# Performance work log

Hardware: AMD Instinct MI355X
Metric: run time of the kernel (lower is better)

Reference implementation:

```python
import jax, jax.numpy as jnp
import numpy as np

B, T, D = 2, 1024, 1024
H, DK = 16, 64  # n_head, d_k; inner dim = H*DK = D
INV_SQRT_DK = 1.0 / float(np.sqrt(DK))


def setup_inputs() -> dict:
    key = jax.random.key(0)
    ks = jax.random.split(key, 16)
    init = lambda k, shape: (jax.random.normal(k, shape, dtype=jnp.float32) * 0.02)
    return {
        "query": jax.random.normal(ks[0], (B, T, D), dtype=jnp.float32),
        "key": jax.random.normal(ks[1], (B, T, D), dtype=jnp.float32),
        "value": jax.random.normal(ks[2], (B, T, D), dtype=jnp.float32),
        "pos_k": jax.random.normal(ks[3], (T, T, DK), dtype=jnp.float32),
        "pos_v": jax.random.normal(ks[4], (T, T, DK), dtype=jnp.float32),
        "mask": jnp.ones((B, T, T), dtype=jnp.int32),
        "relative_attention_bias": jax.random.normal(ks[5], (1, H, T, T), dtype=jnp.float32),
        "Wq": init(ks[6], (D, D)), "bq": init(ks[7], (D,)),
        "Wk": init(ks[8], (D, D)), "bk": init(ks[9], (D,)),
        "Wv": init(ks[10], (D, D)), "bv": init(ks[11], (D,)),
        "Wo": init(ks[12], (D, D)), "bo": init(ks[13], (D,)),
    }


def reference(query, key, value, pos_k, pos_v, mask, relative_attention_bias,
              Wq, bq, Wk, bk, Wv, bv, Wo, bo):
    nb = query.shape[0]
    # projections -> (B, H, T, DK); q pre-scaled by 1/sqrt(d_k)
    q = (query @ Wq + bq).reshape(nb, -1, H, DK).transpose(0, 2, 1, 3) * INV_SQRT_DK
    k = (key @ Wk + bk).reshape(nb, -1, H, DK).transpose(0, 2, 1, 3)
    v = (value @ Wv + bv).reshape(nb, -1, H, DK).transpose(0, 2, 1, 3)

    # content scores + relative-position key scores (B, H, T, S)
    A = jnp.einsum('bhtd,bhsd->bhts', q, k)
    Bp = jnp.einsum('bhtd,tsd->bhts', q, pos_k)
    scores = A + Bp + relative_attention_bias

    # masked softmax: mask (B, T, S) -> invalid where mask == 0
    inv = (mask[:, None, :, :] == 0)  # (B, 1, T, S)
    scores = jnp.where(inv, -jnp.inf, scores)
    attn = jax.nn.softmax(scores, axis=-1)
    attn = jnp.where(inv, 0.0, attn)

    # value aggregation + relative-position value term
    x = jnp.einsum('bhts,bhsd->bhtd', attn, v)
    x = x + jnp.einsum('bhts,tsd->bhtd', attn, pos_v)

    x = x.transpose(0, 2, 1, 3).reshape(nb, -1, H * DK)  # (B, T, D)
    return x @ Wo + bo
```

## Files before the change

### kernel.cpp

```cpp
#include <hip/hip_runtime.h>


#define DEV __device__ __forceinline__

typedef short bf16x8 __attribute__((ext_vector_type(8)));
typedef float f32x4 __attribute__((ext_vector_type(4)));

DEV short f2b(float f) {
  unsigned u = __builtin_bit_cast(unsigned, f);
  u = (u + 0x7FFFu + ((u >> 16) & 1u)) >> 16;
  return (short)u;
}
DEV float b2f(short s) {
  unsigned u = ((unsigned)(unsigned short)s) << 16;
  return __builtin_bit_cast(float, u);
}

#define MFMA(a, b, c) __builtin_amdgcn_mfma_f32_16x16x32_bf16(a, b, c, 0, 0, 0)

DEV void gload16(const void* g, void* l) {
  __builtin_amdgcn_global_load_lds(
      (const __attribute__((address_space(1))) void*)g,
      (__attribute__((address_space(3))) void*)l, 16, 0, 0);
}

__global__ __launch_bounds__(256) void k_cvt3(
    const float* __restrict__ a, const float* __restrict__ b, const float* __restrict__ c,
    short* __restrict__ oa, short* __restrict__ ob, short* __restrict__ oc) {
  const float* src = blockIdx.y == 0 ? a : (blockIdx.y == 1 ? b : c);
  short* dst = blockIdx.y == 0 ? oa : (blockIdx.y == 1 ? ob : oc);
  size_t i = ((size_t)blockIdx.x * 256 + threadIdx.x) * 8;
  float4 p0 = *(const float4*)(src + i);
  float4 p1 = *(const float4*)(src + i + 4);
  bf16x8 o;
  o[0] = f2b(p0.x); o[1] = f2b(p0.y); o[2] = f2b(p0.z); o[3] = f2b(p0.w);
  o[4] = f2b(p1.x); o[5] = f2b(p1.y); o[6] = f2b(p1.z); o[7] = f2b(p1.w);
  *(bf16x8*)(dst + i) = o;
}

__global__ __launch_bounds__(256) void k_wtrans4(
    const float* __restrict__ w0, const float* __restrict__ w1,
    const float* __restrict__ w2, const float* __restrict__ w3,
    short* __restrict__ o0, short* __restrict__ o1,
    short* __restrict__ o2, short* __restrict__ o3) {
  const float* src; short* dst;
  switch (blockIdx.z) {
    case 0: src = w0; dst = o0; break;
    case 1: src = w1; dst = o1; break;
    case 2: src = w2; dst = o2; break;
    default: src = w3; dst = o3;
  }
  __shared__ short LW[64][74];
  const int tid = threadIdx.x;
  const int k0 = blockIdx.y * 64, n0 = blockIdx.x * 64;
  {
    int c4 = (tid & 15) * 4;
#pragma unroll
    for (int i = 0; i < 4; ++i) {
      int r = (tid >> 4) + i * 16;
      float4 v = *(const float4*)(src + (size_t)(k0 + r) * 1024 + n0 + c4);
      LW[r][c4 + 0] = f2b(v.x); LW[r][c4 + 1] = f2b(v.y);
      LW[r][c4 + 2] = f2b(v.z); LW[r][c4 + 3] = f2b(v.w);
    }
  }
  __syncthreads();
  {
    int n = tid >> 2, kb = (tid & 3) * 16;
#pragma unroll
    for (int j2 = 0; j2 < 2; ++j2) {
      int kk = kb + j2 * 8;
      bf16x8 o;
#pragma unroll
      for (int j = 0; j < 8; ++j) o[j] = LW[kk + j][n];
      *(bf16x8*)(dst + (size_t)(n0 + n) * 1024 + k0 + kk) = o;
    }
  }
}

__global__ __launch_bounds__(256) void k_qkv(
    const short* __restrict__ Ain, const short* __restrict__ WT,
    const float* __restrict__ bq, const float* __restrict__ bk,
    const float* __restrict__ bv,
    short* __restrict__ qo, short* __restrict__ ko, short* __restrict__ vTo) {
  __shared__ short As[128 * 32];
  __shared__ short Bs[128 * 32];
  __shared__ short LW[128][136];
  const int tid = threadIdx.x;
  const int w = tid >> 6, l = tid & 63, lg = l >> 4, lr = l & 15;
  const int wm = w >> 1, wn = w & 1;
  const int n0 = blockIdx.x * 128;
  const int m0 = blockIdx.y * 128;
  const int seg = m0 >> 11;
  const int mseg = m0 & 2047;
  const short* Abase = Ain + ((size_t)m0 << 10);
  const short* Bbase = WT + ((size_t)seg << 20) + ((size_t)n0 << 10);
  const int srow = l >> 2, scol8 = (l & 3) * 8;
  f32x4 acc[4][4] = {};
  for (int k0 = 0; k0 < 1024; k0 += 32) {
#pragma unroll
    for (int c = 0; c < 2; ++c) {
      int chunk = w * 2 + c;
      int row = chunk * 16 + srow;
      gload16(Abase + (size_t)row * 1024 + k0 + scol8, &As[chunk * 512]);
      gload16(Bbase + (size_t)row * 1024 + k0 + scol8, &Bs[chunk * 512]);
    }
    __syncthreads();
    bf16x8 af[4], bf[4];
#pragma unroll
    for (int i = 0; i < 4; ++i) af[i] = *(const bf16x8*)&As[(wm * 64 + i * 16 + lr) * 32 + lg * 8];
#pragma unroll
    for (int i = 0; i < 4; ++i) bf[i] = *(const bf16x8*)&Bs[(wn * 64 + i * 16 + lr) * 32 + lg * 8];
#pragma unroll
    for (int mi = 0; mi < 4; ++mi)
#pragma unroll
      for (int ni = 0; ni < 4; ++ni) acc[mi][ni] = MFMA(af[mi], bf[ni], acc[mi][ni]);
    __syncthreads();
  }
  const float* bias = seg == 0 ? bq : (seg == 1 ? bk : bv);
  const float scale = seg == 0 ? 0.125f : 1.0f;
  float bvals[4];
#pragma unroll
  for (int ni = 0; ni < 4; ++ni) bvals[ni] = bias[n0 + wn * 64 + ni * 16 + lr];
#pragma unroll
  for (int mi = 0; mi < 4; ++mi)
#pragma unroll
    for (int ni = 0; ni < 4; ++ni)
#pragma unroll
      for (int r = 0; r < 4; ++r)
        LW[wm * 64 + mi * 16 + lg * 4 + r][wn * 64 + ni * 16 + lr] =
            f2b((acc[mi][ni][r] + bvals[ni]) * scale);
  __syncthreads();
  if (seg < 2) {
    short* dst = seg == 0 ? qo : ko;
    int r = tid >> 1, half = tid & 1;
    int m = mseg + r, b = m >> 10, t = m & 1023;
#pragma unroll
    for (int g = 0; g < 8; ++g) {
      int n = n0 + half * 64 + g * 8;
      int h = n >> 6, dk = n & 63;
      bf16x8 o = *(const bf16x8*)&LW[r][half * 64 + g * 8];
      *(bf16x8*)(dst + (((size_t)(b * 16 + h) * 1024 + t) << 6) + dk) = o;
    }
  } else {
    int dkc = tid & 127, th = tid >> 7;
    int n = n0 + dkc, h = n >> 6, dk = n & 63;
    int b = mseg >> 10;
    int tbase = (mseg & 1023) + th * 64;
#pragma unroll
    for (int g = 0; g < 8; ++g) {
      bf16x8 o;
#pragma unroll
      for (int e = 0; e < 8; ++e) o[e] = LW[th * 64 + g * 8 + e][dkc];
      *(bf16x8*)(vTo + (((size_t)(b * 16 + h) * 64 + dk) << 10) + tbase + g * 8) = o;
    }
  }
}

__global__ __launch_bounds__(256) void k_posk_bias(
    const short* __restrict__ q, const float* __restrict__ pos_k,
    const float* __restrict__ rab, const int* __restrict__ mask,
    short* __restrict__ S) {
  const int t = blockIdx.y;
  const int tid = threadIdx.x;
  const int w = tid >> 6, l = tid & 63, lg = l >> 4, lr = l & 15;
  const int s0 = blockIdx.x * 256 + w * 64;
  __shared__ short LW[4][32][74];
  bf16x8 af[2][2];
#pragma unroll
  for (int mi = 0; mi < 2; ++mi)
#pragma unroll
    for (int kk = 0; kk < 2; ++kk) {
      int bh = mi * 16 + lr;
      af[mi][kk] = *(const bf16x8*)(q + ((size_t)bh * 1024 + t) * 64 + kk * 32 + lg * 8);
    }
  f32x4 acc[2][4] = {};
#pragma unroll
  for (int ni = 0; ni < 4; ++ni) {
    int s = s0 + ni * 16 + lr;
#pragma unroll
    for (int kk = 0; kk < 2; ++kk) {
      const float* pk = pos_k + ((size_t)t * 1024 + s) * 64 + kk * 32 + lg * 8;
      const float4 p0 = *(const float4*)pk;
      const float4 p1 = *(const float4*)(pk + 4);
      bf16x8 bfr;
      bfr[0] = f2b(p0.x); bfr[1] = f2b(p0.y); bfr[2] = f2b(p0.z); bfr[3] = f2b(p0.w);
      bfr[4] = f2b(p1.x); bfr[5] = f2b(p1.y); bfr[6] = f2b(p1.z); bfr[7] = f2b(p1.w);
#pragma unroll
      for (int mi = 0; mi < 2; ++mi) acc[mi][ni] = MFMA(af[mi][kk], bfr, acc[mi][ni]);
    }
  }
#pragma unroll
  for (int ni = 0; ni < 4; ++ni) {
    int s = s0 + ni * 16 + lr;
    int msk0 = mask[(size_t)t * 1024 + s];
    int msk1 = mask[(size_t)(1024 + t) * 1024 + s];
#pragma unroll
    for (int r = 0; r < 4; ++r) {
      int h = lg * 4 + r;
      float bv = rab[((size_t)h * 1024 + t) * 1024 + s];
      float v0 = acc[0][ni][r] + bv;
      float v1 = acc[1][ni][r] + bv;
      if (msk0 == 0) v0 = -1e30f;
      if (msk1 == 0) v1 = -1e30f;
      LW[w][h][ni * 16 + lr] = f2b(v0);
      LW[w][16 + h][ni * 16 + lr] = f2b(v1);
    }
  }
#pragma unroll
  for (int rr = 0; rr < 4; ++rr) {
    int row = (l >> 3) + rr * 8;
    int s8 = (l & 7) * 8;
    bf16x8 o = *(const bf16x8*)&LW[w][row][s8];
    *(bf16x8*)(S + ((size_t)row * 1024 + t) * 1024 + s0 + s8) = o;
  }
}

__global__ __launch_bounds__(512, 4) void k_attn_softmax(
    const short* __restrict__ q, const short* __restrict__ kmat,
    short* __restrict__ S) {
  const int bh = blockIdx.y;
  const int tid = threadIdx.x;
  const int w = tid >> 6, l = tid & 63, lg = l >> 4, lr = l & 15;
  const int wm = w >> 2, wn = w & 3;
  const int t0 = blockIdx.x * 32 + wm * 16;
  const int scol = wn * 256;
  __shared__ short LS[8][16][266];
  __shared__ float redA[32][4];
  __shared__ float redB[32][4];

  short* sb = (short*)(S + ((size_t)bh * 1024 + t0) * 1024 + scol);
  const int r2 = l >> 5, c16 = (l & 31) * 8;
#pragma unroll
  for (int rr = 0; rr < 8; ++rr) {
    int row = rr * 2 + r2;
    *(bf16x8*)&LS[w][row][c16] = *(const bf16x8*)(sb + (size_t)row * 1024 + c16);
  }

  bf16x8 af[2];
#pragma unroll
  for (int kk = 0; kk < 2; ++kk)
    af[kk] = *(const bf16x8*)(q + ((size_t)bh * 1024 + (t0 + lr)) * 64 + kk * 32 + lg * 8);

  f32x4 acc[16];
#pragma unroll
  for (int ni = 0; ni < 16; ++ni) {
    int s = scol + ni * 16 + lr;
    const short* kp = kmat + ((size_t)bh * 1024 + s) * 64 + lg * 8;
    bf16x8 b0 = *(const bf16x8*)kp;
    bf16x8 b1 = *(const bf16x8*)(kp + 32);
    f32x4 a = {};
    a = MFMA(af[0], b0, a);
    a = MFMA(af[1], b1, a);
    acc[ni] = a;
  }
#pragma unroll
  for (int ni = 0; ni < 16; ++ni)
#pragma unroll
    for (int r = 0; r < 4; ++r) acc[ni][r] += b2f(LS[w][lg * 4 + r][ni * 16 + lr]);

  float pm[4];
#pragma unroll
  for (int r = 0; r < 4; ++r) {
    float m = acc[0][r];
#pragma unroll
    for (int ni = 1; ni < 16; ++ni) m = fmaxf(m, acc[ni][r]);
    m = fmaxf(m, __shfl_xor(m, 1));
    m = fmaxf(m, __shfl_xor(m, 2));
    m = fmaxf(m, __shfl_xor(m, 4));
    m = fmaxf(m, __shfl_xor(m, 8));
    pm[r] = m;
  }
  if (lr == 0) {
#pragma unroll
    for (int r = 0; r < 4; ++r) redA[wm * 16 + lg * 4 + r][wn] = pm[r];
  }
  __syncthreads();
  float rowm[4];
#pragma unroll
  for (int r = 0; r < 4; ++r) {
    int row = wm * 16 + lg * 4 + r;
    rowm[r] = fmaxf(fmaxf(redA[row][0], redA[row][1]), fmaxf(redA[row][2], redA[row][3]));
  }
  float rs[4];
#pragma unroll
  for (int r = 0; r < 4; ++r) {
    float sum = 0.f;
#pragma unroll
    for (int ni = 0; ni < 16; ++ni) {
      float e = __expf(acc[ni][r] - rowm[r]);
      acc[ni][r] = e;
      sum += e;
    }
    sum += __shfl_xor(sum, 1);
    sum += __shfl_xor(sum, 2);
    sum += __shfl_xor(sum, 4);
    sum += __shfl_xor(sum, 8);
    rs[r] = sum;
  }
  if (lr == 0) {
#pragma unroll
    for (int r = 0; r < 4; ++r) redB[wm * 16 + lg * 4 + r][wn] = rs[r];
  }
  __syncthreads();
#pragma unroll
  for (int r = 0; r < 4; ++r) {
    int row = wm * 16 + lg * 4 + r;
    float inv = 1.0f / (redB[row][0] + redB[row][1] + redB[row][2] + redB[row][3]);
#pragma unroll
    for (int ni = 0; ni < 16; ++ni) LS[w][lg * 4 + r][ni * 16 + lr] = f2b(acc[ni][r] * inv);
  }
#pragma unroll
  for (int rr = 0; rr < 8; ++rr) {
    int row = rr * 2 + r2;
    bf16x8 o = *(const bf16x8*)&LS[w][row][c16];
    *(bf16x8*)(sb + (size_t)row * 1024 + c16) = o;
  }
}

__global__ __launch_bounds__(256) void k_posv(
    const short* __restrict__ S, const float* __restrict__ pos_v,
    short* __restrict__ X0h) {
  const int t = blockIdx.x;
  const int tid = threadIdx.x;
  const int w = tid >> 6, l = tid & 63, lg = l >> 4, lr = l & 15;
  const int mi = w >> 1;
  const int nb = (w & 1) * 2;
  __shared__ short pv[256][66];
  f32x4 acc[2] = {};
  const int srow = tid >> 4;
  const int dk4 = (tid & 15) * 4;
  for (int c = 0; c < 4; ++c) {
    int sc = c * 256;
    if (c) __syncthreads();
#pragma unroll
    for (int it = 0; it < 16; ++it) {
      int s = srow + it * 16;
      float4 p = *(const float4*)(pos_v + ((size_t)t * 1024 + sc + s) * 64 + dk4);
      unsigned p0 = (unsigned)(unsigned short)f2b(p.x) | ((unsigned)(unsigned short)f2b(p.y) << 16);
      unsigned p1 = (unsigned)(unsigned short)f2b(p.z) | ((unsigned)(unsigned short)f2b(p.w) << 16);
      *(unsigned*)&pv[s][dk4] = p0;
      *(unsigned*)&pv[s][dk4 + 2] = p1;
    }
    __syncthreads();
    const int bh = mi * 16 + lr;
#pragma unroll
    for (int kk = 0; kk < 8; ++kk) {
      bf16x8 afr = *(const bf16x8*)(S + ((size_t)bh * 1024 + t) * 1024 + sc + kk * 32 + lg * 8);
#pragma unroll
      for (int ni = 0; ni < 2; ++ni) {
        int dk = (nb + ni) * 16 + lr;
        bf16x8 bfr;
#pragma unroll
        for (int j = 0; j < 8; ++j) bfr[j] = pv[kk * 32 + lg * 8 + j][dk];
        acc[ni] = MFMA(afr, bfr, acc[ni]);
      }
    }
  }
#pragma unroll
  for (int ni = 0; ni < 2; ++ni)
#pragma unroll
    for (int r = 0; r < 4; ++r) {
      int bh = mi * 16 + lg * 4 + r;
      int b = bh >> 4, h = bh & 15;
      int dk = (nb + ni) * 16 + lr;
      X0h[((size_t)(b * 1024 + t)) * 1024 + h * 64 + dk] = f2b(acc[ni][r]);
    }
}

__global__ __launch_bounds__(256) void k_av(
    const short* __restrict__ S, const short* __restrict__ vT,
    const short* __restrict__ X0h, short* __restrict__ X) {
  const int bh = blockIdx.y;
  const int tt0 = blockIdx.x * 128;
  const int tid = threadIdx.x;
  const int w = tid >> 6, l = tid & 63, lg = l >> 4, lr = l & 15;
  const short* vbase = vT + ((size_t)bh << 16);
  const short* sbase = S + ((size_t)bh << 20);
  f32x4 acc[2][4] = {};
#pragma unroll 4
  for (int kk = 0; kk < 32; ++kk) {
    bf16x8 afr[2];
#pragma unroll
    for (int mi = 0; mi < 2; ++mi) {
      int tt = tt0 + (w * 2 + mi) * 16 + lr;
      afr[mi] = *(const bf16x8*)(sbase + ((size_t)tt << 10) + kk * 32 + lg * 8);
    }
#pragma unroll
    for (int ni = 0; ni < 4; ++ni) {
      bf16x8 bfr = *(const bf16x8*)(vbase + ((ni * 16 + lr) << 10) + kk * 32 + lg * 8);
#pragma unroll
      for (int mi = 0; mi < 2; ++mi) acc[mi][ni] = MFMA(afr[mi], bfr, acc[mi][ni]);
    }
  }
  const int b = bh >> 4, h = bh & 15;
#pragma unroll
  for (int mi = 0; mi < 2; ++mi)
#pragma unroll
    for (int ni = 0; ni < 4; ++ni)
#pragma unroll
      for (int r = 0; r < 4; ++r) {
        int tt = tt0 + (w * 2 + mi) * 16 + lg * 4 + r;
        int d = h * 64 + ni * 16 + lr;
        size_t idx = ((size_t)(b * 1024 + tt)) * 1024 + d;
        X[idx] = f2b(b2f(X0h[idx]) + acc[mi][ni][r]);
      }
}

__global__ __launch_bounds__(256) void k_oproj(
    const short* __restrict__ X, const short* __restrict__ WT,
    const float* __restrict__ bias, float* __restrict__ out) {
  __shared__ short As[128 * 32];
  __shared__ short Bs[128 * 32];
  const int tid = threadIdx.x;
  const int w = tid >> 6, l = tid & 63, lg = l >> 4, lr = l & 15;
  const int wm = w >> 1, wn = w & 1;
  const int n0 = blockIdx.x * 128;
  const int m0 = blockIdx.y * 128;
  const short* Abase = X + ((size_t)m0 << 10);
  const short* Bbase = WT + ((size_t)n0 << 10);
  const int srow = l >> 2, scol8 = (l & 3) * 8;
  f32x4 acc[4][4] = {};
  for (int k0 = 0; k0 < 1024; k0 += 32) {
#pragma unroll
    for (int c = 0; c < 2; ++c) {
      int chunk = w * 2 + c;
      int row = chunk * 16 + srow;
      gload16(Abase + (size_t)row * 1024 + k0 + scol8, &As[chunk * 512]);
      gload16(Bbase + (size_t)row * 1024 + k0 + scol8, &Bs[chunk * 512]);
    }
    __syncthreads();
    bf16x8 af[4], bf[4];
#pragma unroll
    for (int i = 0; i < 4; ++i) af[i] = *(const bf16x8*)&As[(wm * 64 + i * 16 + lr) * 32 + lg * 8];
#pragma unroll
    for (int i = 0; i < 4; ++i) bf[i] = *(const bf16x8*)&Bs[(wn * 64 + i * 16 + lr) * 32 + lg * 8];
#pragma unroll
    for (int mi = 0; mi < 4; ++mi)
#pragma unroll
      for (int ni = 0; ni < 4; ++ni) acc[mi][ni] = MFMA(af[mi], bf[ni], acc[mi][ni]);
    __syncthreads();
  }
  float bvals[4];
#pragma unroll
  for (int ni = 0; ni < 4; ++ni) bvals[ni] = bias[n0 + wn * 64 + ni * 16 + lr];
#pragma unroll
  for (int mi = 0; mi < 4; ++mi)
#pragma unroll
    for (int ni = 0; ni < 4; ++ni)
#pragma unroll
      for (int r = 0; r < 4; ++r) {
        int m = m0 + wm * 64 + mi * 16 + lg * 4 + r;
        int n = n0 + wn * 64 + ni * 16 + lr;
        out[(size_t)m * 1024 + n] = acc[mi][ni][r] + bvals[ni];
      }
}

extern "C" void kernel_launch(void* const* d_in, const int* in_sizes, int n_in,
                              void* d_out, int out_size, void* d_ws, size_t ws_size,
                              hipStream_t stream) {
  (void)in_sizes; (void)n_in; (void)out_size; (void)ws_size;
  const float* query = (const float*)d_in[0];
  const float* key   = (const float*)d_in[1];
  const float* value = (const float*)d_in[2];
  const float* pos_k = (const float*)d_in[3];
  const float* pos_v = (const float*)d_in[4];
  const int*   mask  = (const int*)d_in[5];
  const float* rab   = (const float*)d_in[6];
  const float* Wq = (const float*)d_in[7];
  const float* bq = (const float*)d_in[8];
  const float* Wk = (const float*)d_in[9];
  const float* bk = (const float*)d_in[10];
  const float* Wv = (const float*)d_in[11];
  const float* bv = (const float*)d_in[12];
  const float* Wo = (const float*)d_in[13];
  const float* bo = (const float*)d_in[14];
  float* out = (float*)d_out;

  const size_t M2 = 2ull * 1024 * 1024;
  short* q   = (short*)d_ws;
  short* k   = q + M2;
  short* vT  = k + M2;
  short* S   = vT + M2;
  short* X0h = S + 32ull * 1024 * 1024;
  short* X   = X0h + M2;
  short* qin = X + M2;
  short* kin = qin + M2;
  short* vin = kin + M2;
  short* WqT = vin + M2;
  short* WkT = WqT + 1024 * 1024;
  short* WvT = WkT + 1024 * 1024;
  short* WoT = WvT + 1024 * 1024;

  k_cvt3<<<dim3(1024, 3), dim3(256), 0, stream>>>(query, key, value, qin, kin, vin);
  k_wtrans4<<<dim3(16, 16, 4), dim3(256), 0, stream>>>(Wq, Wk, Wv, Wo, WqT, WkT, WvT, WoT);
  k_qkv<<<dim3(8, 48), dim3(256), 0, stream>>>(qin, WqT, bq, bk, bv, q, k, vT);
  k_posk_bias<<<dim3(4, 1024), dim3(256), 0, stream>>>(q, pos_k, rab, mask, S);
  k_attn_softmax<<<dim3(32, 32), dim3(512), 0, stream>>>(q, k, S);
  k_posv<<<dim3(1024), dim3(256), 0, stream>>>(S, pos_v, X0h);
  k_av<<<dim3(8, 32), dim3(256), 0, stream>>>(S, vT, X0h, X);
  k_oproj<<<dim3(8, 16), dim3(256), 0, stream>>>(X, WoT, bo, out);
}
```

Before: 307.1 us.

## Shrink GEMM tiles for more blocks and stage bias/mask via LDS

The QKV, AV and output-projection kernels get smaller output tiles (64-wide N, 32-row AV blocks, 64x64 oproj), which raises the grid sizes so more blocks fill the many CUs. The posk_bias kernel now loads the relative bias and mask rows into shared memory with coalesced float4/int4 reads instead of scattered per-lane global loads. The softmax kernel's launch-bounds occupancy hint drops from 4 to 2, which gives the compiler more registers per thread. Smaller tiles mean less data reuse per block and more global traffic in exchange for the added parallelism.

```diff
diff --git a/kernel.cpp b/kernel.cpp
--- a/kernel.cpp
+++ b/kernel.cpp
@@ -83,74 +83,70 @@
     const float* __restrict__ bv,
     short* __restrict__ qo, short* __restrict__ ko, short* __restrict__ vTo) {
   __shared__ short As[128 * 32];
-  __shared__ short Bs[128 * 32];
-  __shared__ short LW[128][136];
+  __shared__ short Bs[64 * 32];
+  __shared__ short LW[128][72];
   const int tid = threadIdx.x;
   const int w = tid >> 6, l = tid & 63, lg = l >> 4, lr = l & 15;
   const int wm = w >> 1, wn = w & 1;
-  const int n0 = blockIdx.x * 128;
+  const int n0 = blockIdx.x * 64;
   const int m0 = blockIdx.y * 128;
   const int seg = m0 >> 11;
   const int mseg = m0 & 2047;
   const short* Abase = Ain + ((size_t)m0 << 10);
   const short* Bbase = WT + ((size_t)seg << 20) + ((size_t)n0 << 10);
   const int srow = l >> 2, scol8 = (l & 3) * 8;
-  f32x4 acc[4][4] = {};
+  f32x4 acc[4][2] = {};
   for (int k0 = 0; k0 < 1024; k0 += 32) {
-#pragma unroll
-    for (int c = 0; c < 2; ++c) {
-      int chunk = w * 2 + c;
-      int row = chunk * 16 + srow;
-      gload16(Abase + (size_t)row * 1024 + k0 + scol8, &As[chunk * 512]);
-      gload16(Bbase + (size_t)row * 1024 + k0 + scol8, &Bs[chunk * 512]);
-    }
+    gload16(Abase + (size_t)((w * 2) * 16 + srow) * 1024 + k0 + scol8, &As[(w * 2) * 512]);
+    gload16(Abase + (size_t)((w * 2 + 1) * 16 + srow) * 1024 + k0 + scol8, &As[(w * 2 + 1) * 512]);
+    gload16(Bbase + (size_t)(w * 16 + srow) * 1024 + k0 + scol8, &Bs[w * 512]);
     __syncthreads();
-    bf16x8 af[4], bf[4];
+    bf16x8 af[4], bf[2];
 #pragma unroll
     for (int i = 0; i < 4; ++i) af[i] = *(const bf16x8*)&As[(wm * 64 + i * 16 + lr) * 32 + lg * 8];
 #pragma unroll
-    for (int i = 0; i < 4; ++i) bf[i] = *(const bf16x8*)&Bs[(wn * 64 + i * 16 + lr) * 32 + lg * 8];
+    for (int i = 0; i < 2; ++i) bf[i] = *(const bf16x8*)&Bs[(wn * 32 + i * 16 + lr) * 32 + lg * 8];
 #pragma unroll
     for (int mi = 0; mi < 4; ++mi)
 #pragma unroll
-      for (int ni = 0; ni < 4; ++ni) acc[mi][ni] = MFMA(af[mi], bf[ni], acc[mi][ni]);
+      for (int ni = 0; ni < 2; ++ni) acc[mi][ni] = MFMA(af[mi], bf[ni], acc[mi][ni]);
     __syncthreads();
   }
   const float* bias = seg == 0 ? bq : (seg == 1 ? bk : bv);
   const float scale = seg == 0 ? 0.125f : 1.0f;
-  float bvals[4];
-#pragma unroll
-  for (int ni = 0; ni < 4; ++ni) bvals[ni] = bias[n0 + wn * 64 + ni * 16 + lr];
+  float bvals[2];
+#pragma unroll
+  for (int ni = 0; ni < 2; ++ni) bvals[ni] = bias[n0 + wn * 32 + ni * 16 + lr];
 #pragma unroll
   for (int mi = 0; mi < 4; ++mi)
 #pragma unroll
-    for (int ni = 0; ni < 4; ++ni)
+    for (int ni = 0; ni < 2; ++ni)
 #pragma unroll
       for (int r = 0; r < 4; ++r)
-        LW[wm * 64 + mi * 16 + lg * 4 + r][wn * 64 + ni * 16 + lr] =
+        LW[wm * 64 + mi * 16 + lg * 4 + r][wn * 32 + ni * 16 + lr] =
             f2b((acc[mi][ni][r] + bvals[ni]) * scale);
   __syncthreads();
   if (seg < 2) {
     short* dst = seg == 0 ? qo : ko;
     int r = tid >> 1, half = tid & 1;
     int m = mseg + r, b = m >> 10, t = m & 1023;
-#pragma unroll
-    for (int g = 0; g < 8; ++g) {
-      int n = n0 + half * 64 + g * 8;
-      int h = n >> 6, dk = n & 63;
-      bf16x8 o = *(const bf16x8*)&LW[r][half * 64 + g * 8];
+    int h = n0 >> 6;
+#pragma unroll
+    for (int g = 0; g < 4; ++g) {
+      int dk = half * 32 + g * 8;
+      bf16x8 o = *(const bf16x8*)&LW[r][dk];
       *(bf16x8*)(dst + (((size_t)(b * 16 + h) * 1024 + t) << 6) + dk) = o;
     }
   } else {
-    int dkc = tid & 127, th = tid >> 7;
-    int n = n0 + dkc, h = n >> 6, dk = n & 63;
+    int dkc = tid & 63, th = tid >> 6;
+    int h = n0 >> 6, dk = dkc;
     int b = mseg >> 10;
-    int tbase = (mseg & 1023) + th * 64;
-#pragma unroll
-    for (int g = 0; g < 8; ++g) {
+    int tbase = (mseg & 1023) + th * 32;
+#pragma unroll
+    for (int g = 0; g < 4; ++g) {
       bf16x8 o;
 #pragma unroll
-      for (int e = 0; e < 8; ++e) o[e] = LW[th * 64 + g * 8 + e][dkc];
+      for (int e = 0; e < 8; ++e) o[e] = LW[th * 32 + g * 8 + e][dkc];
       *(bf16x8*)(vTo + (((size_t)(b * 16 + h) * 64 + dk) << 10) + tbase + g * 8) = o;
     }
   }
@@ -163,8 +159,25 @@
   const int t = blockIdx.y;
   const int tid = threadIdx.x;
   const int w = tid >> 6, l = tid & 63, lg = l >> 4, lr = l & 15;
-  const int s0 = blockIdx.x * 256 + w * 64;
+  const int sB = blockIdx.x * 256;
+  const int s0 = sB + w * 64;
+  __shared__ float RB[16][260];
+  __shared__ int MK[2][260];
   __shared__ short LW[4][32][74];
+  {
+    int hr = tid >> 4, c0 = (tid & 15) * 4;
+#pragma unroll
+    for (int it = 0; it < 4; ++it) {
+      int c = c0 + it * 64;
+      float4 v = *(const float4*)(rab + ((size_t)hr * 1024 + t) * 1024 + sB + c);
+      RB[hr][c] = v.x; RB[hr][c + 1] = v.y; RB[hr][c + 2] = v.z; RB[hr][c + 3] = v.w;
+    }
+  }
+  if (tid < 128) {
+    int br = tid >> 6, c = (tid & 63) * 4;
+    int4 mv = *(const int4*)(mask + ((size_t)br * 1024 + t) * 1024 + sB + c);
+    MK[br][c] = mv.x; MK[br][c + 1] = mv.y; MK[br][c + 2] = mv.z; MK[br][c + 3] = mv.w;
+  }
   bf16x8 af[2][2];
 #pragma unroll
   for (int mi = 0; mi < 2; ++mi)
@@ -189,15 +202,16 @@
       for (int mi = 0; mi < 2; ++mi) acc[mi][ni] = MFMA(af[mi][kk], bfr, acc[mi][ni]);
     }
   }
+  __syncthreads();
 #pragma unroll
   for (int ni = 0; ni < 4; ++ni) {
-    int s = s0 + ni * 16 + lr;
-    int msk0 = mask[(size_t)t * 1024 + s];
-    int msk1 = mask[(size_t)(1024 + t) * 1024 + s];
+    int colw = w * 64 + ni * 16 + lr;
+    int msk0 = MK[0][colw];
+    int msk1 = MK[1][colw];
 #pragma unroll
     for (int r = 0; r < 4; ++r) {
       int h = lg * 4 + r;
-      float bv = rab[((size_t)h * 1024 + t) * 1024 + s];
+      float bv = RB[h][colw];
       float v0 = acc[0][ni][r] + bv;
       float v1 = acc[1][ni][r] + bv;
       if (msk0 == 0) v0 = -1e30f;
@@ -215,7 +229,7 @@
   }
 }
 
-__global__ __launch_bounds__(512, 4) void k_attn_softmax(
+__global__ __launch_bounds__(512, 2) void k_attn_softmax(
     const short* __restrict__ q, const short* __restrict__ kmat,
     short* __restrict__ S) {
   const int bh = blockIdx.y;
@@ -371,86 +385,74 @@
     const short* __restrict__ S, const short* __restrict__ vT,
     const short* __restrict__ X0h, short* __restrict__ X) {
   const int bh = blockIdx.y;
-  const int tt0 = blockIdx.x * 128;
+  const int tt0 = blockIdx.x * 32;
   const int tid = threadIdx.x;
   const int w = tid >> 6, l = tid & 63, lg = l >> 4, lr = l & 15;
-  const short* vbase = vT + ((size_t)bh << 16);
-  const short* sbase = S + ((size_t)bh << 20);
-  f32x4 acc[2][4] = {};
-#pragma unroll 4
+  const int wm = w >> 1, wn = w & 1;
+  const short* vbase = vT + ((size_t)bh << 16) + ((size_t)(wn * 32) << 10);
+  const short* sbase = S + ((size_t)bh << 20) + ((size_t)(tt0 + wm * 16) << 10);
+  f32x4 acc[2] = {};
+#pragma unroll 8
   for (int kk = 0; kk < 32; ++kk) {
-    bf16x8 afr[2];
-#pragma unroll
-    for (int mi = 0; mi < 2; ++mi) {
-      int tt = tt0 + (w * 2 + mi) * 16 + lr;
-      afr[mi] = *(const bf16x8*)(sbase + ((size_t)tt << 10) + kk * 32 + lg * 8);
-    }
-#pragma unroll
-    for (int ni = 0; ni < 4; ++ni) {
-      bf16x8 bfr = *(const bf16x8*)(vbase + ((ni * 16 + lr) << 10) + kk * 32 + lg * 8);
-#pragma unroll
-      for (int mi = 0; mi < 2; ++mi) acc[mi][ni] = MFMA(afr[mi], bfr, acc[mi][ni]);
+    bf16x8 afr = *(const bf16x8*)(sbase + ((size_t)lr << 10) + kk * 32 + lg * 8);
+#pragma unroll
+    for (int ni = 0; ni < 2; ++ni) {
+      bf16x8 bfr = *(const bf16x8*)(vbase + ((size_t)(ni * 16 + lr) << 10) + kk * 32 + lg * 8);
+      acc[ni] = MFMA(afr, bfr, acc[ni]);
     }
   }
   const int b = bh >> 4, h = bh & 15;
 #pragma unroll
-  for (int mi = 0; mi < 2; ++mi)
-#pragma unroll
-    for (int ni = 0; ni < 4; ++ni)
-#pragma unroll
-      for (int r = 0; r < 4; ++r) {
-        int tt = tt0 + (w * 2 + mi) * 16 + lg * 4 + r;
-        int d = h * 64 + ni * 16 + lr;
-        size_t idx = ((size_t)(b * 1024 + tt)) * 1024 + d;
-        X[idx] = f2b(b2f(X0h[idx]) + acc[mi][ni][r]);
-      }
+  for (int ni = 0; ni < 2; ++ni)
+#pragma unroll
+    for (int r = 0; r < 4; ++r) {
+      int tt = tt0 + wm * 16 + lg * 4 + r;
+      int d = h * 64 + wn * 32 + ni * 16 + lr;
+      size_t idx = ((size_t)(b * 1024 + tt)) * 1024 + d;
+      X[idx] = f2b(b2f(X0h[idx]) + acc[ni][r]);
+    }
 }
 
 __global__ __launch_bounds__(256) void k_oproj(
     const short* __restrict__ X, const short* __restrict__ WT,
     const float* __restrict__ bias, float* __restrict__ out) {
-  __shared__ short As[128 * 32];
-  __shared__ short Bs[128 * 32];
+  __shared__ short As[64 * 32];
+  __shared__ short Bs[64 * 32];
   const int tid = threadIdx.x;
   const int w = tid >> 6, l = tid & 63, lg = l >> 4, lr = l & 15;
   const int wm = w >> 1, wn = w & 1;
-  const int n0 = blockIdx.x * 128;
-  const int m0 = blockIdx.y * 128;
+  const int n0 = blockIdx.x * 64;
+  const int m0 = blockIdx.y * 64;
   const short* Abase = X + ((size_t)m0 << 10);
   const short* Bbase = WT + ((size_t)n0 << 10);
   const int srow = l >> 2, scol8 = (l & 3) * 8;
-  f32x4 acc[4][4] = {};
+  f32x4 acc[2][2] = {};
   for (int k0 = 0; k0 < 1024; k0 += 32) {
-#pragma unroll
-    for (int c = 0; c < 2; ++c) {
-      int chunk = w * 2 + c;
-      int row = chunk * 16 + srow;
-      gload16(Abase + (size_t)row * 1024 + k0 + scol8, &As[chunk * 512]);
-      gload16(Bbase + (size_t)row * 1024 + k0 + scol8, &Bs[chunk * 512]);
-    }
+    gload16(Abase + (size_t)(w * 16 + srow) * 1024 + k0 + scol8, &As[w * 512]);
+    gload16(Bbase + (size_t)(w * 16 + srow) * 1024 + k0 + scol8, &Bs[w * 512]);
     __syncthreads();
-    bf16x8 af[4], bf[4];
-#pragma unroll
-    for (int i = 0; i < 4; ++i) af[i] = *(const bf16x8*)&As[(wm * 64 + i * 16 + lr) * 32 + lg * 8];
-#pragma unroll
-    for (int i = 0; i < 4; ++i) bf[i] = *(const bf16x8*)&Bs[(wn * 64 + i * 16 + lr) * 32 + lg * 8];
-#pragma unroll
-    for (int mi = 0; mi < 4; ++mi)
-#pragma unroll
-      for (int ni = 0; ni < 4; ++ni) acc[mi][ni] = MFMA(af[mi], bf[ni], acc[mi][ni]);
+    bf16x8 af[2], bf[2];
+#pragma unroll
+    for (int i = 0; i < 2; ++i) af[i] = *(const bf16x8*)&As[(wm * 32 + i * 16 + lr) * 32 + lg * 8];
+#pragma unroll
+    for (int i = 0; i < 2; ++i) bf[i] = *(const bf16x8*)&Bs[(wn * 32 + i * 16 + lr) * 32 + lg * 8];
+#pragma unroll
+    for (int mi = 0; mi < 2; ++mi)
+#pragma unroll
+      for (int ni = 0; ni < 2; ++ni) acc[mi][ni] = MFMA(af[mi], bf[ni], acc[mi][ni]);
     __syncthreads();
   }
-  float bvals[4];
-#pragma unroll
-  for (int ni = 0; ni < 4; ++ni) bvals[ni] = bias[n0 + wn * 64 + ni * 16 + lr];
-#pragma unroll
-  for (int mi = 0; mi < 4; ++mi)
-#pragma unroll
-    for (int ni = 0; ni < 4; ++ni)
+  float bvals[2];
+#pragma unroll
+  for (int ni = 0; ni < 2; ++ni) bvals[ni] = bias[n0 + wn * 32 + ni * 16 + lr];
+#pragma unroll
+  for (int mi = 0; mi < 2; ++mi)
+#pragma unroll
+    for (int ni = 0; ni < 2; ++ni)
 #pragma unroll
       for (int r = 0; r < 4; ++r) {
-        int m = m0 + wm * 64 + mi * 16 + lg * 4 + r;
-        int n = n0 + wn * 64 + ni * 16 + lr;
+        int m = m0 + wm * 32 + mi * 16 + lg * 4 + r;
+        int n = n0 + wn * 32 + ni * 16 + lr;
         out[(size_t)m * 1024 + n] = acc[mi][ni][r] + bvals[ni];
       }
 }
@@ -493,10 +495,10 @@
 
   k_cvt3<<<dim3(1024, 3), dim3(256), 0, stream>>>(query, key, value, qin, kin, vin);
   k_wtrans4<<<dim3(16, 16, 4), dim3(256), 0, stream>>>(Wq, Wk, Wv, Wo, WqT, WkT, WvT, WoT);
-  k_qkv<<<dim3(8, 48), dim3(256), 0, stream>>>(qin, WqT, bq, bk, bv, q, k, vT);
+  k_qkv<<<dim3(16, 48), dim3(256), 0, stream>>>(qin, WqT, bq, bk, bv, q, k, vT);
   k_posk_bias<<<dim3(4, 1024), dim3(256), 0, stream>>>(q, pos_k, rab, mask, S);
   k_attn_softmax<<<dim3(32, 32), dim3(512), 0, stream>>>(q, k, S);
   k_posv<<<dim3(1024), dim3(256), 0, stream>>>(S, pos_v, X0h);
-  k_av<<<dim3(8, 32), dim3(256), 0, stream>>>(S, vT, X0h, X);
-  k_oproj<<<dim3(8, 16), dim3(256), 0, stream>>>(X, WoT, bo, out);
-}
+  k_av<<<dim3(32, 32), dim3(256), 0, stream>>>(S, vT, X0h, X);
+  k_oproj<<<dim3(16, 32), dim3(256), 0, stream>>>(X, WoT, bo, out);
+}
```

Result: no change. 307.7 us (+0.2%).
